# Kernel tuning notes

Hardware: AMD Instinct MI355X
Metric: run time of the kernel (lower is better)

## Reference

```python
import jax, jax.numpy as jnp
import numpy as np

B, F, E, C = 2048, 39, 64, 64  # batch, num_fields, embed_dim, conv_size


def setup_inputs() -> dict:
    key = jax.random.key(0)
    k1, k2, k3 = jax.random.split(key, 3)
    x_emb = jax.random.normal(k1, (B, F, E), dtype=jnp.float32)
    # Conv2d(1, C, (2, E), (2, 1)) weight: (C, 1, 2, E), bias: (C,)
    W = jax.random.normal(k2, (C, 1, 2, E), dtype=jnp.float32) * 0.05
    b = jax.random.normal(k3, (C,), dtype=jnp.float32) * 0.05
    return {"x_emb": x_emb, "W": W, "b": b}


def reference(x_emb, W, b):
    Bn, Fn, En = x_emb.shape
    # All C(F,2) ordered pairs (i<j), same order as the python double loop
    ii, jj = np.triu_indices(Fn, k=1)  # each length P
    xi = x_emb[:, ii]  # (B, P, E)
    xj = x_emb[:, jj]  # (B, P, E)
    # kernel (2, E) with stride (2, 1) over the stacked (2P, E) map is a
    # shared linear over each pair: y[b,p,c] = xi.Wi[c] + xj.Wj[c] + bias[c]
    Wi = W[:, 0, 0, :]  # (C, E)
    Wj = W[:, 0, 1, :]  # (C, E)
    y = jnp.einsum('bpe,ce->bpc', xi, Wi) + jnp.einsum('bpe,ce->bpc', xj, Wj) + b
    y = jax.nn.relu(y)  # (B, P, C)
    # torch conv output is (B, C, P, 1) contiguous; .view(B, -1, C) reshapes
    # that C-major buffer into (B, P, C) WITHOUT transposing -> replicate exactly
    Cn = y.shape[-1]
    out = jnp.transpose(y, (0, 2, 1)).reshape(Bn, -1, Cn)
    return out
```

## Files before the change

### kernel.cpp

```cpp
#include <hip/hip_runtime.h>


#define BATCH 2048
#define FDIM  39
#define EDIM  64
#define CDIM  64
#define NPAIR 741
#define XSTR  40
#define WSTR  132
#define ASTR  41

__global__ __launch_bounds__(256) void interconv_fused(
    const float* __restrict__ x,
    const float* __restrict__ Wg,
    const float* __restrict__ bias,
    float* __restrict__ out)
{
    __shared__ float smem[EDIM * XSTR + EDIM * WSTR];
    __shared__ int   tab[NPAIR];
    __shared__ float sbias[CDIM];

    float* xT = smem;
    float* Wl = smem + EDIM * XSTR;
    float* A  = smem;

    const int tid = threadIdx.x;
    const int b   = blockIdx.x;
    const float* xg = x + (size_t)b * (FDIM * EDIM);

    for (int q = tid; q < (FDIM * EDIM) / 4; q += 256) {
        float4 v = ((const float4*)xg)[q];
        int flat = q << 2;
        int f  = flat >> 6;
        int e0 = flat & 63;
        xT[(e0 + 0) * XSTR + f] = v.x;
        xT[(e0 + 1) * XSTR + f] = v.y;
        xT[(e0 + 2) * XSTR + f] = v.z;
        xT[(e0 + 3) * XSTR + f] = v.w;
    }
    for (int q = tid; q < (CDIM * 2 * EDIM) / 4; q += 256) {
        float4 v = ((const float4*)Wg)[q];
        int flat = q << 2;
        int c   = flat >> 7;
        int rem = flat & 127;
        int wh  = rem >> 6;
        int e0  = rem & 63;
        int cw  = (wh << 6) | c;
        Wl[(e0 + 0) * WSTR + cw] = v.x;
        Wl[(e0 + 1) * WSTR + cw] = v.y;
        Wl[(e0 + 2) * WSTR + cw] = v.z;
        Wl[(e0 + 3) * WSTR + cw] = v.w;
    }
    for (int idx = tid; idx < NPAIR; idx += 256) {
        int i = (int)floorf((77.0f - sqrtf(5929.0f - 8.0f * (float)idx)) * 0.5f);
        i = i < 0 ? 0 : (i > FDIM - 2 ? FDIM - 2 : i);
        while ((i + 1) * (77 - (i + 1)) / 2 <= idx) ++i;
        while (i * (77 - i) / 2 > idx) --i;
        int j = idx - i * (77 - i) / 2 + i + 1;
        tab[idx] = i | (j << 8);
    }
    if (tid < CDIM) sbias[tid] = bias[tid];
    __syncthreads();

    const int ft  = tid >> 5;
    const int ct  = tid & 31;
    const int f0  = ft * 5;
    const int cw0 = ct * 4;

    float acc[5][4];
#pragma unroll
    for (int a = 0; a < 5; ++a)
#pragma unroll
        for (int q = 0; q < 4; ++q) acc[a][q] = 0.0f;

#pragma unroll 4
    for (int e = 0; e < EDIM; ++e) {
        float4 wv = *(const float4*)(Wl + e * WSTR + cw0);
        float xv[5];
#pragma unroll
        for (int a = 0; a < 5; ++a) xv[a] = xT[e * XSTR + f0 + a];
#pragma unroll
        for (int a = 0; a < 5; ++a) {
            acc[a][0] = fmaf(xv[a], wv.x, acc[a][0]);
            acc[a][1] = fmaf(xv[a], wv.y, acc[a][1]);
            acc[a][2] = fmaf(xv[a], wv.z, acc[a][2]);
            acc[a][3] = fmaf(xv[a], wv.w, acc[a][3]);
        }
    }
    __syncthreads();

#pragma unroll
    for (int a = 0; a < 5; ++a)
#pragma unroll
        for (int q = 0; q < 4; ++q)
            A[(cw0 + q) * ASTR + (f0 + a)] = acc[a][q];
    __syncthreads();

    float* outb = out + (size_t)b * (CDIM * NPAIR);
    for (int c = 0; c < CDIM; ++c) {
        const float bc = sbias[c];
        const float* rI = A + c * ASTR;
        const float* rJ = A + (64 + c) * ASTR;
        float* oc = outb + c * NPAIR;
        for (int p = tid; p < NPAIR; p += 256) {
            int t = tab[p];
            float v = rI[t & 0xff] + rJ[t >> 8] + bc;
            oc[p] = v > 0.0f ? v : 0.0f;
        }
    }
}

extern "C" void kernel_launch(void* const* d_in, const int* in_sizes, int n_in,
                              void* d_out, int out_size, void* d_ws, size_t ws_size,
                              hipStream_t stream) {
    const float* x    = (const float*)d_in[0];
    const float* W    = (const float*)d_in[1];
    const float* bias = (const float*)d_in[2];
    float* out        = (float*)d_out;

    interconv_fused<<<dim3(BATCH), dim3(256), 0, stream>>>(x, W, bias, out);
}
```

Baseline: 437.0 us.

## Read weights from global, keep x row-major, hoist pair indices into registers

Stops staging the transposed weight matrix and transposed x in shared memory. x is now copied as-is with float4 stores, and weights are read directly from global/L2 as float4 rows inside the GEMM loop, which is vectorised over four e values. The pair-index table is replaced by per-thread registers holding up to three (i,j) pairs, removing the table lookup from the output loop. This reduces LDS footprint and setup cost, but every block re-reads the weights from cache and the x float4 LDS reads may cause bank conflicts.

Measured after the change: 441.7 us. Within noise of the previous version (+1.1%).

```diff
diff --git a/kernel.cpp b/kernel.cpp
--- a/kernel.cpp
+++ b/kernel.cpp
@@ -6,8 +6,6 @@
 #define EDIM  64
 #define CDIM  64
 #define NPAIR 741
-#define XSTR  40
-#define WSTR  132
 #define ASTR  41
 
 __global__ __launch_bounds__(256) void interconv_fused(
@@ -16,56 +14,55 @@
     const float* __restrict__ bias,
     float* __restrict__ out)
 {
-    __shared__ float smem[EDIM * XSTR + EDIM * WSTR];
-    __shared__ int   tab[NPAIR];
+    __shared__ float smem[128 * ASTR];
     __shared__ float sbias[CDIM];
 
-    float* xT = smem;
-    float* Wl = smem + EDIM * XSTR;
+    float* xL = smem;
     float* A  = smem;
 
     const int tid = threadIdx.x;
     const int b   = blockIdx.x;
     const float* xg = x + (size_t)b * (FDIM * EDIM);
 
-    for (int q = tid; q < (FDIM * EDIM) / 4; q += 256) {
-        float4 v = ((const float4*)xg)[q];
-        int flat = q << 2;
-        int f  = flat >> 6;
-        int e0 = flat & 63;
-        xT[(e0 + 0) * XSTR + f] = v.x;
-        xT[(e0 + 1) * XSTR + f] = v.y;
-        xT[(e0 + 2) * XSTR + f] = v.z;
-        xT[(e0 + 3) * XSTR + f] = v.w;
+    for (int q = tid; q < (FDIM * EDIM) / 4; q += 256)
+        ((float4*)xL)[q] = ((const float4*)xg)[q];
+    if (tid < CDIM) sbias[tid] = bias[tid];
+
+    const int  p0   = tid;
+    const int  p1   = tid + 256;
+    const bool has2 = (tid + 512 < NPAIR);
+    const int  p2   = has2 ? tid + 512 : NPAIR - 1;
+    int iv[3], jv[3];
+    {
+        const int pp[3] = {p0, p1, p2};
+#pragma unroll
+        for (int t = 0; t < 3; ++t) {
+            int p = pp[t];
+            int i = (int)floorf((77.0f - sqrtf(static_cast<float>(5929 - 8 * p))) * 0.5f);
+            i = i < 0 ? 0 : (i > FDIM - 2 ? FDIM - 2 : i);
+            while ((i + 1) * (77 - (i + 1)) / 2 <= p) ++i;
+            while (i * (77 - i) / 2 > p) --i;
+            iv[t] = i;
+            jv[t] = p - i * (77 - i) / 2 + i + 1;
+        }
     }
-    for (int q = tid; q < (CDIM * 2 * EDIM) / 4; q += 256) {
-        float4 v = ((const float4*)Wg)[q];
-        int flat = q << 2;
-        int c   = flat >> 7;
-        int rem = flat & 127;
-        int wh  = rem >> 6;
-        int e0  = rem & 63;
-        int cw  = (wh << 6) | c;
-        Wl[(e0 + 0) * WSTR + cw] = v.x;
-        Wl[(e0 + 1) * WSTR + cw] = v.y;
-        Wl[(e0 + 2) * WSTR + cw] = v.z;
-        Wl[(e0 + 3) * WSTR + cw] = v.w;
-    }
-    for (int idx = tid; idx < NPAIR; idx += 256) {
-        int i = (int)floorf((77.0f - sqrtf(5929.0f - 8.0f * (float)idx)) * 0.5f);
-        i = i < 0 ? 0 : (i > FDIM - 2 ? FDIM - 2 : i);
-        while ((i + 1) * (77 - (i + 1)) / 2 <= idx) ++i;
-        while (i * (77 - i) / 2 > idx) --i;
-        int j = idx - i * (77 - i) / 2 + i + 1;
-        tab[idx] = i | (j << 8);
-    }
-    if (tid < CDIM) sbias[tid] = bias[tid];
+    const int i0 = iv[0], j0 = jv[0];
+    const int i1 = iv[1], j1 = jv[1];
+    const int i2 = iv[2], j2 = jv[2];
+
     __syncthreads();
 
     const int ft  = tid >> 5;
     const int ct  = tid & 31;
     const int f0  = ft * 5;
     const int cw0 = ct * 4;
+
+    const float* wrp[4];
+#pragma unroll
+    for (int q = 0; q < 4; ++q) {
+        const int cw = cw0 + q;
+        wrp[q] = Wg + (cw & 63) * 128 + (cw >> 6) * 64;
+    }
 
     float acc[5][4];
 #pragma unroll
@@ -74,39 +71,45 @@
         for (int q = 0; q < 4; ++q) acc[a][q] = 0.0f;
 
 #pragma unroll 4
-    for (int e = 0; e < EDIM; ++e) {
-        float4 wv = *(const float4*)(Wl + e * WSTR + cw0);
-        float xv[5];
-#pragma unroll
-        for (int a = 0; a < 5; ++a) xv[a] = xT[e * XSTR + f0 + a];
+    for (int e0 = 0; e0 < EDIM; e0 += 4) {
+        const float4 w0 = *(const float4*)(wrp[0] + e0);
+        const float4 w1 = *(const float4*)(wrp[1] + e0);
+        const float4 w2 = *(const float4*)(wrp[2] + e0);
+        const float4 w3 = *(const float4*)(wrp[3] + e0);
 #pragma unroll
         for (int a = 0; a < 5; ++a) {
-            acc[a][0] = fmaf(xv[a], wv.x, acc[a][0]);
-            acc[a][1] = fmaf(xv[a], wv.y, acc[a][1]);
-            acc[a][2] = fmaf(xv[a], wv.z, acc[a][2]);
-            acc[a][3] = fmaf(xv[a], wv.w, acc[a][3]);
+            const float4 xv = *(const float4*)(xL + (f0 + a) * EDIM + e0);
+            acc[a][0] = fmaf(xv.w, w0.w, fmaf(xv.z, w0.z, fmaf(xv.y, w0.y, fmaf(xv.x, w0.x, acc[a][0]))));
+            acc[a][1] = fmaf(xv.w, w1.w, fmaf(xv.z, w1.z, fmaf(xv.y, w1.y, fmaf(xv.x, w1.x, acc[a][1]))));
+            acc[a][2] = fmaf(xv.w, w2.w, fmaf(xv.z, w2.z, fmaf(xv.y, w2.y, fmaf(xv.x, w2.x, acc[a][2]))));
+            acc[a][3] = fmaf(xv.w, w3.w, fmaf(xv.z, w3.z, fmaf(xv.y, w3.y, fmaf(xv.x, w3.x, acc[a][3]))));
         }
     }
     __syncthreads();
 
 #pragma unroll
-    for (int a = 0; a < 5; ++a)
+    for (int q = 0; q < 4; ++q)
 #pragma unroll
-        for (int q = 0; q < 4; ++q)
-            A[(cw0 + q) * ASTR + (f0 + a)] = acc[a][q];
+        for (int a = 0; a < 5; ++a)
+            A[(cw0 + q) * ASTR + f0 + a] = acc[a][q];
     __syncthreads();
 
     float* outb = out + (size_t)b * (CDIM * NPAIR);
+    const float* rI = A;
+    const float* rJ = A + 64 * ASTR;
+    float* oc = outb;
+#pragma unroll 2
     for (int c = 0; c < CDIM; ++c) {
         const float bc = sbias[c];
-        const float* rI = A + c * ASTR;
-        const float* rJ = A + (64 + c) * ASTR;
-        float* oc = outb + c * NPAIR;
-        for (int p = tid; p < NPAIR; p += 256) {
-            int t = tab[p];
-            float v = rI[t & 0xff] + rJ[t >> 8] + bc;
-            oc[p] = v > 0.0f ? v : 0.0f;
+        const float v0 = rI[i0] + rJ[j0] + bc;
+        const float v1 = rI[i1] + rJ[j1] + bc;
+        oc[p0] = v0 > 0.0f ? v0 : 0.0f;
+        oc[p1] = v1 > 0.0f ? v1 : 0.0f;
+        if (has2) {
+            const float v2 = rI[i2] + rJ[j2] + bc;
+            oc[p2] = v2 > 0.0f ? v2 : 0.0f;
         }
+        rI += ASTR; rJ += ASTR; oc += NPAIR;
     }
 }
 
```
